# Kernel optimization log

Measured on AMD Instinct MI355X. Metric: run time of the kernel, lower is better.

## Reference

```python
import jax, jax.numpy as jnp
import numpy as np

N_NODES = 200000
N_EDGES = 3200000
HIDDEN = 64
N_GRAPHS = 4096
IN_CH = 2
N_CLASSES = 7


def setup_inputs() -> dict:
    key = jax.random.key(0)
    ks = jax.random.split(key, 12)
    x = jax.random.normal(ks[0], (N_NODES, IN_CH), dtype=jnp.float32)
    edge_index = jax.random.randint(ks[1], (2, N_EDGES), 0, N_NODES, dtype=jnp.int64)
    batch = jnp.sort(jax.random.randint(ks[2], (N_NODES,), 0, N_GRAPHS, dtype=jnp.int64))
    def glorot(k, shape):
        lim = float(np.sqrt(6.0 / (shape[0] + shape[1])))
        return jax.random.uniform(k, shape, jnp.float32, -lim, lim)
    return {
        'x': x,
        'edge_index': edge_index,
        'batch': batch,
        'W1': glorot(ks[3], (IN_CH, HIDDEN)), 'b1': jnp.zeros((HIDDEN,), jnp.float32),
        'W2': glorot(ks[4], (HIDDEN, HIDDEN)), 'b2': jnp.zeros((HIDDEN,), jnp.float32),
        'W3': glorot(ks[5], (HIDDEN, HIDDEN)), 'b3': jnp.zeros((HIDDEN,), jnp.float32),
        'Wf1': glorot(ks[6], (HIDDEN, HIDDEN)), 'bf1': jnp.zeros((HIDDEN,), jnp.float32),
        'Wf2': glorot(ks[7], (HIDDEN, N_CLASSES)), 'bf2': jnp.zeros((N_CLASSES,), jnp.float32),
    }


def _gcn_layer(x, W, b, src, dst, norm, n_nodes):
    # GCNConv: out = sum_{(s,d)} norm_sd * (x W)[s] scattered to d, plus bias
    xw = x @ W  # [N, H]
    msgs = norm[:, None] * xw[src]  # gather over edges (incl. self-loops)
    out = jax.ops.segment_sum(msgs, dst, num_segments=n_nodes)
    return out + b


def _gcn_norm(edge_index, n_nodes):
    # add self-loops, symmetric normalization D^-1/2 (A+I) D^-1/2
    loops = jnp.arange(n_nodes, dtype=edge_index.dtype)
    src = jnp.concatenate([edge_index[0], loops])
    dst = jnp.concatenate([edge_index[1], loops])
    deg = jax.ops.segment_sum(jnp.ones_like(dst, dtype=jnp.float32), dst, num_segments=n_nodes)
    dinv = jnp.where(deg > 0, jax.lax.rsqrt(jnp.maximum(deg, 1.0)), 0.0)
    norm = dinv[src] * dinv[dst]
    return src, dst, norm


def reference(x, edge_index, batch, W1, b1, W2, b2, W3, b3, Wf1, bf1, Wf2, bf2):
    n_nodes = x.shape[0]
    src, dst, norm = _gcn_norm(edge_index, n_nodes)
    h = jax.nn.relu(_gcn_layer(x, W1, b1, src, dst, norm, n_nodes))
    h = jax.nn.relu(_gcn_layer(h, W2, b2, src, dst, norm, n_nodes))
    h = jax.nn.relu(_gcn_layer(h, W3, b3, src, dst, norm, n_nodes))
    # global mean pool over graphs
    sums = jax.ops.segment_sum(h, batch, num_segments=N_GRAPHS)
    counts = jax.ops.segment_sum(jnp.ones((n_nodes,), jnp.float32), batch, num_segments=N_GRAPHS)
    pooled = sums / jnp.maximum(counts, 1.0)[:, None]
    # MLP head (dropout inactive in eval)
    hid = jax.nn.relu(pooled @ Wf1 + bf1)
    return hid @ Wf2 + bf2
```

## Files before the change

### kernel.cpp

```cpp
#include <hip/hip_runtime.h>
#include <hip/hip_fp16.h>

#define N_NODES  200000
#define N_EDGES  3200000
#define HIDDEN   64
#define N_GRAPHS 4096
#define N_CLASSES 7
#define NBUCK    196
#define BSHIFT   10
#define BMASK    1023
#define CPW      16
#define NCHUNK   (N_NODES / CPW)
#define GLAYER   (NCHUNK / 4)

#define CH_EPT 16
__global__ void k_chist(const int* __restrict__ dst, int* __restrict__ chist) {
    __shared__ int h[NBUCK];
    for (int i = threadIdx.x; i < NBUCK; i += 256) h[i] = 0;
    __syncthreads();
    int base = blockIdx.x * 256 * CH_EPT + threadIdx.x;
    for (int k = 0; k < CH_EPT; ++k) {
        int e = base + k * 256;
        if (e < N_EDGES) atomicAdd(&h[dst[e] >> BSHIFT], 1);
    }
    __syncthreads();
    for (int i = threadIdx.x; i < NBUCK; i += 256) atomicAdd(&chist[i], h[i]);
}

__global__ void k_cscan(const int* __restrict__ chist, int* __restrict__ cbase,
                        int* __restrict__ gcur) {
    __shared__ int tmp[256];
    int tid = threadIdx.x;
    int v = (tid < NBUCK) ? chist[tid] : 0;
    int x = v; tmp[tid] = x; __syncthreads();
    for (int o = 1; o < 256; o <<= 1) {
        int y = (tid >= o) ? tmp[tid - o] : 0;
        __syncthreads();
        x += y; tmp[tid] = x;
        __syncthreads();
    }
    if (tid < NBUCK) { cbase[tid] = x - v; gcur[tid] = x - v; }
    if (tid == 0) cbase[NBUCK] = N_EDGES;
}

#define PT_EPT 32
__global__ void k_part(const int* __restrict__ src, const int* __restrict__ dst,
                       int* __restrict__ gcur, int* __restrict__ stage) {
    __shared__ int lh[NBUCK];
    __shared__ int lbase[NBUCK];
    __shared__ int lcur[NBUCK];
    for (int i = threadIdx.x; i < NBUCK; i += 256) { lh[i] = 0; lcur[i] = 0; }
    __syncthreads();
    int base = blockIdx.x * 256 * PT_EPT + threadIdx.x;
    for (int k = 0; k < PT_EPT; ++k) {
        int e = base + k * 256;
        if (e < N_EDGES) atomicAdd(&lh[dst[e] >> BSHIFT], 1);
    }
    __syncthreads();
    for (int i = threadIdx.x; i < NBUCK; i += 256)
        if (lh[i] > 0) lbase[i] = atomicAdd(&gcur[i], lh[i]);
    __syncthreads();
    for (int k = 0; k < PT_EPT; ++k) {
        int e = base + k * 256;
        if (e < N_EDGES) {
            int d = dst[e], b = d >> BSHIFT;
            int lp = atomicAdd(&lcur[b], 1);
            stage[lbase[b] + lp] = (src[e] << BSHIFT) | (d & BMASK);
        }
    }
}

__global__ void k_sort(const int* __restrict__ stage, const int* __restrict__ cbase,
                       int* __restrict__ edges, int* __restrict__ off,
                       int* __restrict__ endv, float* __restrict__ dinv,
                       const float2* __restrict__ x2, float2* __restrict__ xs2) {
    __shared__ int hist[1024];
    __shared__ int tmp[256];
    int b = blockIdx.x, tid = threadIdx.x;
    int cb0 = cbase[b], cb1 = cbase[b + 1];
    for (int k = 0; k < 4; ++k) hist[tid * 4 + k] = 0;
    __syncthreads();
    for (int j = cb0 + tid; j < cb1; j += 256)
        atomicAdd(&hist[stage[j] & BMASK], 1);
    __syncthreads();
    int c0 = hist[tid*4], c1 = hist[tid*4+1], c2 = hist[tid*4+2], c3 = hist[tid*4+3];
    int s = c0 + c1 + c2 + c3;
    int x = s; tmp[tid] = x; __syncthreads();
    for (int o = 1; o < 256; o <<= 1) {
        int y = (tid >= o) ? tmp[tid - o] : 0;
        __syncthreads();
        x += y; tmp[tid] = x;
        __syncthreads();
    }
    int run = x - s;
    int nbase = b << BSHIFT;
    int counts[4] = {c0, c1, c2, c3};
    for (int k = 0; k < 4; ++k) {
        int v = tid * 4 + k;
        hist[v] = run;
        int node = nbase + v;
        if (node < N_NODES) {
            off[node]  = cb0 + run;
            endv[node] = cb0 + run + counts[k];
            float di = rsqrtf((float)counts[k] + 1.0f);
            dinv[node] = di;
            float2 xv = x2[node];
            xs2[node] = make_float2(di * xv.x, di * xv.y);
        }
        run += counts[k];
    }
    __syncthreads();
    for (int j = cb0 + tid; j < cb1; j += 256) {
        int p = stage[j];
        int pos = atomicAdd(&hist[p & BMASK], 1);
        edges[cb0 + pos] = p >> BSHIFT;
    }
}

static __device__ __forceinline__ float rdlf(float v, int l) {
    return __uint_as_float(__builtin_amdgcn_readlane(__float_as_uint(v), (unsigned)l));
}
static __device__ __forceinline__ int rdli(int v, int l) {
    return __builtin_amdgcn_readlane(v, (unsigned)l);
}
static __device__ __forceinline__ void acc4h(float4& a, uint2 r) {
    __half2 h01 = *reinterpret_cast<const __half2*>(&r.x);
    __half2 h23 = *reinterpret_cast<const __half2*>(&r.y);
    float2 f01 = __half22float2(h01);
    float2 f23 = __half22float2(h23);
    a.x += f01.x; a.y += f01.y; a.z += f23.x; a.w += f23.y;
}

__global__ __launch_bounds__(256, 4)
void k_l1(const int* __restrict__ edges, const int* __restrict__ off,
          const int* __restrict__ endv, const float* __restrict__ dinv,
          const float2* __restrict__ xs2,
          const float* __restrict__ W1, const float* __restrict__ b1,
          const float* __restrict__ W2, __half* __restrict__ Yout) {
    int lane = threadIdx.x & 63;
    int wid = blockIdx.x * 4 + (threadIdx.x >> 6);
    int n0 = wid * CPW;
    if (n0 >= N_NODES) return;
    float w1a = W1[lane], w1b = W1[64 + lane], bb = b1[lane];
    float4 wc[16];
#pragma unroll
    for (int t = 0; t < 16; ++t) {
        wc[t].x = W2[(4 * t + 0) * 64 + lane];
        wc[t].y = W2[(4 * t + 1) * 64 + lane];
        wc[t].z = W2[(4 * t + 2) * 64 + lane];
        wc[t].w = W2[(4 * t + 3) * 64 + lane];
    }
#pragma unroll
    for (int t = 0; t < 16; ++t) {
        asm volatile("" : "+v"(wc[t].x), "+v"(wc[t].y), "+v"(wc[t].z), "+v"(wc[t].w));
    }
    int mo = 0, me = 0; float md = 0.0f; float sxx = 0.0f, sxy = 0.0f;
    if (lane < CPW) {
        int nn = n0 + lane;
        mo = off[nn]; me = endv[nn]; md = dinv[nn];
        float2 sv = xs2[nn];
        sxx = sv.x; sxy = sv.y;
    }
    int j0 = rdli(mo, 0);
    int idx = j0 + lane; if (idx > N_EDGES - 1) idx = N_EDGES - 1;
    int ev = edges[idx];
    for (int i = 0; i < CPW; ++i) {
        int n = n0 + i;
        int j1 = rdli(me, i);
        float dn = rdlf(md, i);
        int deg = j1 - j0;
        int evn = 0; int j0n = 0;
        if (i < CPW - 1) {
            j0n = rdli(mo, i + 1);
            int idn = j0n + lane; if (idn > N_EDGES - 1) idn = N_EDGES - 1;
            evn = edges[idn];
        }
        float px = 0.0f, py = 0.0f;
        if (lane < deg) {
            float2 v = xs2[ev];
            px = v.x; py = v.y;
        }
        for (int jj = j0 + 64 + lane; jj < j1; jj += 64) {
            float2 v = xs2[edges[jj]];
            px += v.x; py += v.y;
        }
#pragma unroll
        for (int o = 1; o < 64; o <<= 1) {
            px += __shfl_xor(px, o, 64);
            py += __shfl_xor(py, o, 64);
        }
        float gx = dn * (px + rdlf(sxx, i));
        float gy = dn * (py + rdlf(sxy, i));
        float h = gx * w1a + gy * w1b + bb;
        h = h > 0.0f ? h : 0.0f;
        float y0 = 0.0f, y1 = 0.0f, y2 = 0.0f, y3 = 0.0f;
#pragma unroll
        for (int t = 0; t < 16; ++t) {
            float4 w = wc[t];
            y0 = fmaf(rdlf(h, 4 * t + 0), w.x, y0);
            y1 = fmaf(rdlf(h, 4 * t + 1), w.y, y1);
            y2 = fmaf(rdlf(h, 4 * t + 2), w.z, y2);
            y3 = fmaf(rdlf(h, 4 * t + 3), w.w, y3);
        }
        Yout[n * 64 + lane] = __float2half(dn * ((y0 + y1) + (y2 + y3)));
        ev = evn; j0 = j0n;
    }
}

template<bool FINAL>
__global__ __launch_bounds__(256, 4)
void k_gl(const int* __restrict__ edges, const int* __restrict__ off,
          const int* __restrict__ endv, const float* __restrict__ dinv,
          const __half* __restrict__ Yin, const float* __restrict__ Wn,
          const float* __restrict__ bias, void* __restrict__ Yout) {
    const uint2* __restrict__ Yin2 = (const uint2*)Yin;
    int lane = threadIdx.x & 63;
    int q = lane & 15, s = lane >> 4;
    int wid = blockIdx.x * 4 + (threadIdx.x >> 6);
    int n0 = wid * CPW;
    if (n0 >= N_NODES) return;
    float bb = bias[lane];
    float4 wc[16];
    if (!FINAL) {
#pragma unroll
        for (int t = 0; t < 16; ++t) {
            wc[t].x = Wn[(4 * t + 0) * 64 + lane];
            wc[t].y = Wn[(4 * t + 1) * 64 + lane];
            wc[t].z = Wn[(4 * t + 2) * 64 + lane];
            wc[t].w = Wn[(4 * t + 3) * 64 + lane];
        }
#pragma unroll
        for (int t = 0; t < 16; ++t) {
            asm volatile("" : "+v"(wc[t].x), "+v"(wc[t].y), "+v"(wc[t].z), "+v"(wc[t].w));
        }
    }
    int mo = 0, me = 0; float md = 0.0f;
    if (lane < CPW) {
        int nn = n0 + lane;
        mo = off[nn]; me = endv[nn]; md = dinv[nn];
    }
    int j0 = rdli(mo, 0);
    int j1 = rdli(me, 0);
    int m0 = j1 - j0; if (m0 > 64) m0 = 64;
    int idx = j0 + lane; if (idx > N_EDGES - 1) idx = N_EDGES - 1;
    int ev = edges[idx];
    uint2 sraw = make_uint2(0u, 0u);
    if (s == 0) sraw = Yin2[(size_t)n0 * 16 + q];
    uint2 r0 = make_uint2(0u, 0u), r1 = r0, r2 = r0, r3 = r0;
    uint2 r4 = r0, r5 = r0, r6 = r0, r7 = r0;
    {
        int i0 = __shfl(ev, 0 + s, 64);
        int i1 = __shfl(ev, 4 + s, 64);
        int i2 = __shfl(ev, 8 + s, 64);
        int i3 = __shfl(ev, 12 + s, 64);
        int i4 = __shfl(ev, 16 + s, 64);
        int i5 = __shfl(ev, 20 + s, 64);
        int i6 = __shfl(ev, 24 + s, 64);
        int i7 = __shfl(ev, 28 + s, 64);
        if (m0 > 0)  r0 = Yin2[(size_t)i0 * 16 + q];
        if (m0 > 4)  r1 = Yin2[(size_t)i1 * 16 + q];
        if (m0 > 8)  r2 = Yin2[(size_t)i2 * 16 + q];
        if (m0 > 12) r3 = Yin2[(size_t)i3 * 16 + q];
        if (m0 > 16) r4 = Yin2[(size_t)i4 * 16 + q];
        if (m0 > 20) r5 = Yin2[(size_t)i5 * 16 + q];
        if (m0 > 24) r6 = Yin2[(size_t)i6 * 16 + q];
        if (m0 > 28) r7 = Yin2[(size_t)i7 * 16 + q];
    }
    for (int i = 0; i < CPW; ++i) {
        int n = n0 + i;
        float dn = rdlf(md, i);
        int deg = rdli(me, i) - j0;
        int m = m0;
        int evn = 0; int j0n = 0; int mn = 0;
        uint2 srn = make_uint2(0u, 0u);
        if (i < CPW - 1) {
            j0n = rdli(mo, i + 1);
            int j1n = rdli(me, i + 1);
            mn = j1n - j0n; if (mn > 64) mn = 64;
            int idn = j0n + lane; if (idn > N_EDGES - 1) idn = N_EDGES - 1;
            evn = edges[idn];
            if (s == 0) srn = Yin2[(size_t)(n + 1) * 16 + q];
        }
        float4 acc = make_float4(0.f, 0.f, 0.f, 0.f);
        if (s == 0) acc4h(acc, sraw);
        if (0 + s < m)  acc4h(acc, r0);
        if (4 + s < m)  acc4h(acc, r1);
        if (8 + s < m)  acc4h(acc, r2);
        if (12 + s < m) acc4h(acc, r3);
        if (16 + s < m) acc4h(acc, r4);
        if (20 + s < m) acc4h(acc, r5);
        if (24 + s < m) acc4h(acc, r6);
        if (28 + s < m) acc4h(acc, r7);
        for (int t = 8; 4 * t < m; ++t) {
            int sl = 4 * t + s;
            int ii = __shfl(ev, sl, 64);
            uint2 rr = Yin2[(size_t)ii * 16 + q];
            if (sl < m) acc4h(acc, rr);
        }
        for (int jj = 64; jj < deg; ++jj) {
            int sidx = edges[j0 + jj];
            if (s == 0) {
                uint2 rr = Yin2[(size_t)sidx * 16 + q];
                acc4h(acc, rr);
            }
        }
        if (i < CPW - 1) {
            int i0 = __shfl(evn, 0 + s, 64);
            int i1 = __shfl(evn, 4 + s, 64);
            int i2 = __shfl(evn, 8 + s, 64);
            int i3 = __shfl(evn, 12 + s, 64);
            int i4 = __shfl(evn, 16 + s, 64);
            int i5 = __shfl(evn, 20 + s, 64);
            int i6 = __shfl(evn, 24 + s, 64);
            int i7 = __shfl(evn, 28 + s, 64);
            r0 = make_uint2(0u, 0u); r1 = r0; r2 = r0; r3 = r0;
            r4 = r0; r5 = r0; r6 = r0; r7 = r0;
            if (mn > 0)  r0 = Yin2[(size_t)i0 * 16 + q];
            if (mn > 4)  r1 = Yin2[(size_t)i1 * 16 + q];
            if (mn > 8)  r2 = Yin2[(size_t)i2 * 16 + q];
            if (mn > 12) r3 = Yin2[(size_t)i3 * 16 + q];
            if (mn > 16) r4 = Yin2[(size_t)i4 * 16 + q];
            if (mn > 20) r5 = Yin2[(size_t)i5 * 16 + q];
            if (mn > 24) r6 = Yin2[(size_t)i6 * 16 + q];
            if (mn > 28) r7 = Yin2[(size_t)i7 * 16 + q];
        }
        acc.x += __shfl_xor(acc.x, 16, 64); acc.x += __shfl_xor(acc.x, 32, 64);
        acc.y += __shfl_xor(acc.y, 16, 64); acc.y += __shfl_xor(acc.y, 32, 64);
        acc.z += __shfl_xor(acc.z, 16, 64); acc.z += __shfl_xor(acc.z, 32, 64);
        acc.w += __shfl_xor(acc.w, 16, 64); acc.w += __shfl_xor(acc.w, 32, 64);
        int srcl = lane >> 2;
        float c0 = __shfl(acc.x, srcl, 64);
        float c1 = __shfl(acc.y, srcl, 64);
        float c2 = __shfl(acc.z, srcl, 64);
        float c3 = __shfl(acc.w, srcl, 64);
        float lo = (lane & 1) ? c1 : c0;
        float hi = (lane & 1) ? c3 : c2;
        float sumc = (lane & 2) ? hi : lo;
        float h = dn * sumc + bb;
        h = h > 0.0f ? h : 0.0f;
        if (FINAL) {
            ((float*)Yout)[n * 64 + lane] = h;
        } else {
            float y0 = 0.0f, y1 = 0.0f, y2 = 0.0f, y3 = 0.0f;
#pragma unroll
            for (int t2 = 0; t2 < 16; ++t2) {
                float4 w = wc[t2];
                y0 = fmaf(rdlf(h, 4 * t2 + 0), w.x, y0);
                y1 = fmaf(rdlf(h, 4 * t2 + 1), w.y, y1);
                y2 = fmaf(rdlf(h, 4 * t2 + 2), w.z, y2);
                y3 = fmaf(rdlf(h, 4 * t2 + 3), w.w, y3);
            }
            ((__half*)Yout)[n * 64 + lane] = __float2half(dn * ((y0 + y1) + (y2 + y3)));
        }
        ev = evn; sraw = srn; j0 = j0n; m0 = mn;
    }
}

#define PCHUNK 64
__global__ void k_pool(const float* __restrict__ A, const int* __restrict__ batch,
                       float* __restrict__ sums, float* __restrict__ cnts) {
    int c = threadIdx.x;
    int n0 = blockIdx.x * PCHUNK;
    int n1 = n0 + PCHUNK; if (n1 > N_NODES) n1 = N_NODES;
    int gcur = batch[n0];
    float acc = 0.0f;
    int cnt = 0;
    for (int n = n0; n < n1; ++n) {
        int g = batch[n];
        if (g != gcur) {
            atomicAdd(&sums[gcur * 64 + c], acc);
            if (c == 0) atomicAdd(&cnts[gcur], (float)cnt);
            acc = 0.0f; cnt = 0; gcur = g;
        }
        acc += A[n * 64 + c];
        ++cnt;
    }
    atomicAdd(&sums[gcur * 64 + c], acc);
    if (c == 0) atomicAdd(&cnts[gcur], (float)cnt);
}

__global__ void k_head(const float* __restrict__ sums, const float* __restrict__ cnts,
                       const float* __restrict__ Wf1, const float* __restrict__ bf1,
                       const float* __restrict__ Wf2, const float* __restrict__ bf2,
                       float* __restrict__ out) {
    __shared__ float p[64];
    __shared__ float h[64];
    int g = blockIdx.x;
    int c = threadIdx.x;
    float cnt = cnts[g];
    cnt = cnt > 1.0f ? cnt : 1.0f;
    p[c] = sums[g * 64 + c] / cnt;
    __syncthreads();
    float s = bf1[c];
#pragma unroll
    for (int k = 0; k < 64; ++k) s += p[k] * Wf1[k * 64 + c];
    h[c] = s > 0.0f ? s : 0.0f;
    __syncthreads();
    if (c < N_CLASSES) {
        float o = bf2[c];
#pragma unroll
        for (int k = 0; k < 64; ++k) o += h[k] * Wf2[k * N_CLASSES + c];
        out[g * N_CLASSES + c] = o;
    }
}

extern "C" void kernel_launch(void* const* d_in, const int* in_sizes, int n_in,
                              void* d_out, int out_size, void* d_ws, size_t ws_size,
                              hipStream_t stream) {
    const float* x   = (const float*)d_in[0];
    const int*   ei  = (const int*)d_in[1];
    const int*   bat = (const int*)d_in[2];
    const float* W1  = (const float*)d_in[3];
    const float* b1  = (const float*)d_in[4];
    const float* W2  = (const float*)d_in[5];
    const float* b2  = (const float*)d_in[6];
    const float* W3  = (const float*)d_in[7];
    const float* b3  = (const float*)d_in[8];
    const float* Wf1 = (const float*)d_in[9];
    const float* bf1 = (const float*)d_in[10];
    const float* Wf2 = (const float*)d_in[11];
    const float* bf2 = (const float*)d_in[12];
    float* out = (float*)d_out;

    const int* src = ei;
    const int* dst = ei + N_EDGES;

    char* p = (char*)d_ws;
    float*  A    = (float*)p;   p += (size_t)N_NODES * 64 * 4;
    __half* Ph   = (__half*)p;  p += (size_t)N_NODES * 64 * 2;
    __half* Qh   = (__half*)p;  p += (size_t)N_NODES * 64 * 2;
    int*   stage = (int*)p;     p += (size_t)N_EDGES * 4;
    int*   edges = (int*)p;     p += (size_t)N_EDGES * 4;
    int*   off   = (int*)p;     p += (size_t)N_NODES * 4;
    int*   endv  = (int*)p;     p += (size_t)N_NODES * 4;
    float* dinv  = (float*)p;   p += (size_t)N_NODES * 4;
    float* xs2   = (float*)p;   p += (size_t)N_NODES * 2 * 4;
    int*   chist = (int*)p;     p += (size_t)256 * 4;
    int*   cbase = (int*)p;     p += (size_t)256 * 4;
    int*   gcur  = (int*)p;     p += (size_t)256 * 4;
    float* sums  = (float*)p;   p += (size_t)N_GRAPHS * 64 * 4;
    float* cnts  = (float*)p;   p += (size_t)N_GRAPHS * 4;

    hipMemsetAsync(chist, 0, 256 * 4, stream);
    hipMemsetAsync(sums, 0, (size_t)(N_GRAPHS * 64 + N_GRAPHS) * 4, stream);

    const int BT = 256;
    int gChist = (N_EDGES + 256 * CH_EPT - 1) / (256 * CH_EPT);
    int gPart  = (N_EDGES + 256 * PT_EPT - 1) / (256 * PT_EPT);

    k_chist<<<gChist, BT, 0, stream>>>(dst, chist);
    k_cscan<<<1, 256, 0, stream>>>(chist, cbase, gcur);
    k_part<<<gPart, BT, 0, stream>>>(src, dst, gcur, stage);
    k_sort<<<NBUCK, 256, 0, stream>>>(stage, cbase, edges, off, endv, dinv,
                                      (const float2*)x, (float2*)xs2);

    k_l1<<<GLAYER, BT, 0, stream>>>(edges, off, endv, dinv, (const float2*)xs2,
                                    W1, b1, W2, Ph);

    k_gl<false><<<GLAYER, BT, 0, stream>>>(edges, off, endv, dinv, Ph, W3, b2, Qh);

    k_gl<true><<<GLAYER, BT, 0, stream>>>(edges, off, endv, dinv, Qh, nullptr, b3, A);

    k_pool<<<(N_NODES + PCHUNK - 1) / PCHUNK, 64, 0, stream>>>(A, bat, sums, cnts);
    k_head<<<N_GRAPHS, 64, 0, stream>>>(sums, cnts, Wf1, bf1, Wf2, bf2, out);
}
```

Baseline: 467.0 us.

## Stage partitioned edges in LDS for coalesced writes; prefetch next node's gather in layer 1

The partition kernel now groups each block's edges by bucket in shared memory, using a local prefix scan, and then writes them out contiguously per bucket. This replaces the scattered per-edge global stores. Separately, the first-layer kernel prefetches the next node's first-64-neighbor feature gather one iteration ahead, so gather latency overlaps with the current node's compute. Both changes cost extra LDS (about 40KB per partition block, which lowers occupancy) and extra registers.

```diff
diff --git a/kernel.cpp b/kernel.cpp
--- a/kernel.cpp
+++ b/kernel.cpp
@@ -44,29 +44,53 @@
 }
 
 #define PT_EPT 32
+#define PT_EDGES (256 * PT_EPT)
 __global__ void k_part(const int* __restrict__ src, const int* __restrict__ dst,
                        int* __restrict__ gcur, int* __restrict__ stage) {
     __shared__ int lh[NBUCK];
+    __shared__ int lofs[NBUCK];
     __shared__ int lbase[NBUCK];
     __shared__ int lcur[NBUCK];
-    for (int i = threadIdx.x; i < NBUCK; i += 256) { lh[i] = 0; lcur[i] = 0; }
-    __syncthreads();
-    int base = blockIdx.x * 256 * PT_EPT + threadIdx.x;
+    __shared__ int tmp[256];
+    __shared__ int buf[PT_EDGES];
+    __shared__ unsigned char bid[PT_EDGES];
+    int tid = threadIdx.x;
+    for (int i = tid; i < NBUCK; i += 256) { lh[i] = 0; lcur[i] = 0; }
+    __syncthreads();
+    int base = blockIdx.x * PT_EDGES + tid;
     for (int k = 0; k < PT_EPT; ++k) {
         int e = base + k * 256;
         if (e < N_EDGES) atomicAdd(&lh[dst[e] >> BSHIFT], 1);
     }
     __syncthreads();
-    for (int i = threadIdx.x; i < NBUCK; i += 256)
-        if (lh[i] > 0) lbase[i] = atomicAdd(&gcur[i], lh[i]);
+    int v = (tid < NBUCK) ? lh[tid] : 0;
+    int x = v; tmp[tid] = x; __syncthreads();
+    for (int o = 1; o < 256; o <<= 1) {
+        int y = (tid >= o) ? tmp[tid - o] : 0;
+        __syncthreads();
+        x += y; tmp[tid] = x;
+        __syncthreads();
+    }
+    if (tid < NBUCK) {
+        lofs[tid] = x - v;
+        if (v > 0) lbase[tid] = atomicAdd(&gcur[tid], v);
+    }
     __syncthreads();
     for (int k = 0; k < PT_EPT; ++k) {
         int e = base + k * 256;
         if (e < N_EDGES) {
             int d = dst[e], b = d >> BSHIFT;
-            int lp = atomicAdd(&lcur[b], 1);
-            stage[lbase[b] + lp] = (src[e] << BSHIFT) | (d & BMASK);
-        }
+            int lp = lofs[b] + atomicAdd(&lcur[b], 1);
+            buf[lp] = (src[e] << BSHIFT) | (d & BMASK);
+            bid[lp] = (unsigned char)b;
+        }
+    }
+    __syncthreads();
+    int nval = N_EDGES - blockIdx.x * PT_EDGES;
+    if (nval > PT_EDGES) nval = PT_EDGES;
+    for (int l = tid; l < nval; l += 256) {
+        int b = bid[l];
+        stage[lbase[b] + (l - lofs[b])] = buf[l];
     }
 }
 
@@ -162,25 +186,32 @@
         sxx = sv.x; sxy = sv.y;
     }
     int j0 = rdli(mo, 0);
+    int deg0 = rdli(me, 0) - j0;
     int idx = j0 + lane; if (idx > N_EDGES - 1) idx = N_EDGES - 1;
     int ev = edges[idx];
+    float pxv = 0.0f, pyv = 0.0f;
+    if (lane < deg0) {
+        float2 v = xs2[ev];
+        pxv = v.x; pyv = v.y;
+    }
     for (int i = 0; i < CPW; ++i) {
         int n = n0 + i;
-        int j1 = rdli(me, i);
         float dn = rdlf(md, i);
-        int deg = j1 - j0;
+        int deg = rdli(me, i) - j0;
         int evn = 0; int j0n = 0;
+        float pxn = 0.0f, pyn = 0.0f;
         if (i < CPW - 1) {
             j0n = rdli(mo, i + 1);
+            int degn = rdli(me, i + 1) - j0n;
             int idn = j0n + lane; if (idn > N_EDGES - 1) idn = N_EDGES - 1;
             evn = edges[idn];
-        }
-        float px = 0.0f, py = 0.0f;
-        if (lane < deg) {
-            float2 v = xs2[ev];
-            px = v.x; py = v.y;
-        }
-        for (int jj = j0 + 64 + lane; jj < j1; jj += 64) {
+            if (lane < degn) {
+                float2 v = xs2[evn];
+                pxn = v.x; pyn = v.y;
+            }
+        }
+        float px = pxv, py = pyv;
+        for (int jj = j0 + 64 + lane; jj < j0 + deg; jj += 64) {
             float2 v = xs2[edges[jj]];
             px += v.x; py += v.y;
         }
@@ -203,7 +234,7 @@
             y3 = fmaf(rdlf(h, 4 * t + 3), w.w, y3);
         }
         Yout[n * 64 + lane] = __float2half(dn * ((y0 + y1) + (y2 + y3)));
-        ev = evn; j0 = j0n;
+        ev = evn; j0 = j0n; pxv = pxn; pyv = pyn;
     }
 }
 
@@ -446,7 +477,7 @@
 
     const int BT = 256;
     int gChist = (N_EDGES + 256 * CH_EPT - 1) / (256 * CH_EPT);
-    int gPart  = (N_EDGES + 256 * PT_EPT - 1) / (256 * PT_EPT);
+    int gPart  = (N_EDGES + PT_EDGES - 1) / PT_EDGES;
 
     k_chist<<<gChist, BT, 0, stream>>>(dst, chist);
     k_cscan<<<1, 256, 0, stream>>>(chist, cbase, gcur);
```

Result: no change. 459.6 us (-1.6%).
